# Performance work log

Hardware: AMD Instinct MI355X
Metric: run time of the kernel (lower is better)

The kernel has to match this reference:

```python
import jax, jax.numpy as jnp
import numpy as np

B, T, D = 2, 1024, 1024
H, DH = 16, 64
HD = H * DH          # head_dim = n_heads*d_head = 1024
F = 2048             # expert_dim
E = 8                # n_routed_experts


def bitlinear(x, W):
    # 1.58-bit ternary quant with straight-through estimator
    scale = jnp.clip(jnp.abs(W).mean(axis=1, keepdims=True), 1e-5, None)
    wq = jnp.clip(jnp.round(W / scale), -1.0, 1.0)
    w = W + jax.lax.stop_gradient(wq * scale - W)
    return x @ w.T


def layernorm(x, g, b):
    m = jnp.mean(x, -1, keepdims=True)
    v = jnp.mean((x - m) ** 2, -1, keepdims=True)
    return (x - m) * jax.lax.rsqrt(v + 1e-5) * g + b


def setup_inputs():
    key = jax.random.key(0)
    ks = jax.random.split(key, 12)
    n = lambda k, s, sd: jax.random.normal(k, s, jnp.float32) * sd
    return {
        'x': jax.random.normal(ks[0], (B, T, D), jnp.float32),
        'mask': jnp.tril(jnp.ones((T, T), bool))[None, None],  # causal [1,1,T,T]
        'Wq': n(ks[1], (2 * HD, D), (2 * HD) ** -0.5),
        'Wk': n(ks[2], (2 * HD, D), (2 * HD) ** -0.5),
        'Wv': n(ks[3], (HD, D), HD ** -0.5),
        'Wo': n(ks[4], (D, HD), D ** -0.5),
        'lambda_q': n(ks[5], (H, DH), 0.1),
        'lambda_k': n(ks[6], (H, DH), 0.1),
        'qn_g': jnp.ones(2 * HD), 'qn_b': jnp.zeros(2 * HD),
        'kn_g': jnp.ones(2 * HD), 'kn_b': jnp.zeros(2 * HD),
        'attn_g': jnp.ones(D), 'attn_b': jnp.zeros(D),
        'ffn_g': jnp.ones(D), 'ffn_b': jnp.zeros(D),
        'moe_g': jnp.ones(D), 'moe_b': jnp.zeros(D),
        'shared_w1': n(ks[7], (F, D), F ** -0.5),
        'shared_w2': n(ks[8], (D, F), D ** -0.5),
        'expert_w1': n(ks[9], (E, F, D), F ** -0.5),
        'expert_w2': n(ks[10], (E, D, F), D ** -0.5),
        'router_w': n(ks[11], (E, D), 0.02),
    }


def diff_attention(x, mask, Wq, Wk, Wv, Wo, lambda_q, lambda_k, qn_g, qn_b, kn_g, kn_b):
    Bq, Tq, _ = x.shape
    q = layernorm(bitlinear(x, Wq), qn_g, qn_b).reshape(Bq, Tq, 2, H, DH)
    k = layernorm(bitlinear(x, Wk), kn_g, kn_b).reshape(Bq, Tq, 2, H, DH)
    v = bitlinear(x, Wv).reshape(Bq, Tq, H, DH)
    lam = jnp.clip(jnp.exp(lambda_q.mean() - lambda_k.mean()), 0.1, 2.0)
    scale = DH ** -0.5

    def one_attn(qi, ki):
        s = jnp.einsum('bthd,bshd->bhts', qi, ki) * scale
        s = jnp.where(mask, s, -jnp.inf)
        p = jax.nn.softmax(s, -1)
        return jnp.einsum('bhts,bshd->bthd', p, v)

    out1 = one_attn(q[:, :, 0], k[:, :, 0])
    out2 = one_attn(q[:, :, 1], k[:, :, 1])
    out = (out1 - lam * out2).reshape(Bq, Tq, HD)
    return bitlinear(out, Wo)


def ignition_moe(x, moe_g, moe_b, shared_w1, shared_w2, expert_w1, expert_w2, router_w):
    h = layernorm(x, moe_g, moe_b)
    shared = bitlinear(jax.nn.silu(bitlinear(h, shared_w1)), shared_w2)
    probs = jax.nn.softmax(h @ router_w.T, -1)          # [B,T,E]
    idx = jnp.argmax(probs, -1)                          # top-1 expert id
    top_p = jnp.take_along_axis(probs, idx[..., None], -1)  # [B,T,1]
    routed = jnp.zeros_like(h)
    for e in range(E):  # small fixed expert count
        out_e = bitlinear(jax.nn.silu(bitlinear(h, expert_w1[e])), expert_w2[e])
        sel = (idx == e)[..., None]
        routed = routed + jnp.where(sel, out_e * top_p, 0.0)
    return shared + routed


def reference(x, mask, Wq, Wk, Wv, Wo, lambda_q, lambda_k, qn_g, qn_b, kn_g, kn_b,
              attn_g, attn_b, ffn_g, ffn_b, moe_g, moe_b,
              shared_w1, shared_w2, expert_w1, expert_w2, router_w):
    h = layernorm(x, attn_g, attn_b)
    x = x + diff_attention(h, mask, Wq, Wk, Wv, Wo, lambda_q, lambda_k, qn_g, qn_b, kn_g, kn_b)
    h = layernorm(x, ffn_g, ffn_b)
    x = x + ignition_moe(h, moe_g, moe_b, shared_w1, shared_w2, expert_w1, expert_w2, router_w)
    return x
```

## Files before the change

kernel.cpp:

```cpp
#include <hip/hip_runtime.h>
#include <hip/hip_bf16.h>

#define B_ 2
#define T_ 1024
#define D_ 1024
#define H_ 16
#define DH_ 64
#define F_ 2048
#define E_ 8
#define M_ 2048

typedef _Float16 half8 __attribute__((ext_vector_type(8)));
typedef _Float16 half4v __attribute__((ext_vector_type(4)));
typedef float f32x4 __attribute__((ext_vector_type(4)));

template<bool ABS>
__device__ __forceinline__ float np_pairwise_wave(const float* a, int K, int lane) {
  int nb = K >> 7;
  float s = 0.f;
  if (lane < nb) {
    const float* p = a + (lane << 7);
    float r[8];
    #pragma unroll
    for (int j = 0; j < 8; ++j) r[j] = ABS ? fabsf(p[j]) : p[j];
    for (int i = 8; i < 128; i += 8)
      #pragma unroll
      for (int j = 0; j < 8; ++j) r[j] += ABS ? fabsf(p[i + j]) : p[i + j];
    s = ((r[0] + r[1]) + (r[2] + r[3])) + ((r[4] + r[5]) + (r[6] + r[7]));
  }
  for (int off = 1; off < nb; off <<= 1) s += __shfl_xor(s, off);
  return __shfl(s, 0);
}

__global__ __launch_bounds__(64) void k_scaleq(const float* __restrict__ W, int K,
                                               float* __restrict__ scOut,
                                               _Float16* __restrict__ qOut) {
  int r = blockIdx.x, lane = threadIdx.x;
  const float* row = W + (size_t)r * K;
  float S = np_pairwise_wave<true>(row, K, lane);
  float s = fmaxf(S / (float)K, 1e-5f);
  if (lane == 0) scOut[r] = s;
  _Float16* dst = qOut + (size_t)r * K;
  for (int k = lane * 4; k < K; k += 256) {
    float4 w = *reinterpret_cast<const float4*>(row + k);
    float wv[4] = {w.x, w.y, w.z, w.w};
    half4v q4;
    #pragma unroll
    for (int j = 0; j < 4; ++j) {
      float q = rintf(wv[j] / s);
      q = fminf(1.f, fmaxf(-1.f, q));
      q4[j] = (_Float16)q;
    }
    *reinterpret_cast<half4v*>(dst + k) = q4;
  }
}

__global__ __launch_bounds__(64) void k_lambda(const float* __restrict__ lq,
                                               const float* __restrict__ lk,
                                               float* __restrict__ lam) {
  int lane = threadIdx.x;
  float mq = np_pairwise_wave<false>(lq, 1024, lane) / 1024.0f;
  float mk = np_pairwise_wave<false>(lk, 1024, lane) / 1024.0f;
  if (lane == 0) {
    float l = expf(mq - mk);
    lam[0] = fminf(2.0f, fmaxf(0.1f, l));
  }
}

__global__ __launch_bounds__(256) void k_layernorm(const float* __restrict__ in,
                                                   const float* __restrict__ g,
                                                   const float* __restrict__ b,
                                                   float* __restrict__ out, int Dd) {
  #pragma clang fp contract(off)
  __shared__ float row[2048];
  __shared__ float sq[2048];
  __shared__ float stat[2];
  int m = blockIdx.x, tid = threadIdx.x;
  const float* src = in + (size_t)m * Dd;
  for (int d = tid; d < Dd; d += 256) row[d] = src[d];
  __syncthreads();
  if (tid < 64) {
    float S = np_pairwise_wave<false>(row, Dd, tid);
    if (tid == 0) stat[0] = S;
  }
  __syncthreads();
  float mean = stat[0] / (float)Dd;
  for (int d = tid; d < Dd; d += 256) { float t = row[d] - mean; sq[d] = t * t; }
  __syncthreads();
  if (tid < 64) {
    float S = np_pairwise_wave<false>(sq, Dd, tid);
    if (tid == 0) stat[1] = S;
  }
  __syncthreads();
  float var = stat[1] / (float)Dd;
  float rs = 1.0f / sqrtf(var + 1e-5f);
  float* dst = out + (size_t)m * Dd;
  for (int d = tid; d < Dd; d += 256) {
    float t = row[d] - mean;
    float u = t * rs;
    float v = u * g[d];
    dst[d] = v + b[d];
  }
}

__global__ __launch_bounds__(256) void k_layernorm_split(const float* __restrict__ in,
                                                         const float* __restrict__ g,
                                                         const float* __restrict__ b,
                                                         _Float16* __restrict__ oh,
                                                         _Float16* __restrict__ ol, int Dd) {
  #pragma clang fp contract(off)
  __shared__ float row[2048];
  __shared__ float sq[2048];
  __shared__ float stat[2];
  int m = blockIdx.x, tid = threadIdx.x;
  const float* src = in + (size_t)m * Dd;
  for (int d = tid; d < Dd; d += 256) row[d] = src[d];
  __syncthreads();
  if (tid < 64) {
    float S = np_pairwise_wave<false>(row, Dd, tid);
    if (tid == 0) stat[0] = S;
  }
  __syncthreads();
  float mean = stat[0] / (float)Dd;
  for (int d = tid; d < Dd; d += 256) { float t = row[d] - mean; sq[d] = t * t; }
  __syncthreads();
  if (tid < 64) {
    float S = np_pairwise_wave<false>(sq, Dd, tid);
    if (tid == 0) stat[1] = S;
  }
  __syncthreads();
  float var = stat[1] / (float)Dd;
  float rs = 1.0f / sqrtf(var + 1e-5f);
  #pragma unroll 1
  for (int d = tid; d < Dd; d += 256) {
    float t = row[d] - mean;
    float u = t * rs;
    float v = u * g[d];
    float w = v + b[d];
    _Float16 hv = (_Float16)w;
    oh[(size_t)m * Dd + d] = hv;
    ol[(size_t)m * Dd + d] = (_Float16)((w - (float)hv) * 2048.0f);
  }
}

__global__ __launch_bounds__(256) void k_lnln(const float* __restrict__ in,
                                              const float* __restrict__ g1, const float* __restrict__ b1,
                                              const float* __restrict__ g2, const float* __restrict__ b2,
                                              float* __restrict__ outf,
                                              _Float16* __restrict__ outh) {
  #pragma clang fp contract(off)
  __shared__ float row[1024];
  __shared__ float tmp[1024];
  __shared__ float stat[2];
  int m = blockIdx.x, tid = threadIdx.x;
  const float* src = in + (size_t)m * 1024;
  for (int d = tid; d < 1024; d += 256) row[d] = src[d];
  __syncthreads();
  if (tid < 64) { float S = np_pairwise_wave<false>(row, 1024, tid); if (tid == 0) stat[0] = S; }
  __syncthreads();
  float mean = stat[0] / 1024.0f;
  for (int d = tid; d < 1024; d += 256) { float t = row[d] - mean; tmp[d] = t * t; }
  __syncthreads();
  if (tid < 64) { float S = np_pairwise_wave<false>(tmp, 1024, tid); if (tid == 0) stat[1] = S; }
  __syncthreads();
  float rs = 1.0f / sqrtf(stat[1] / 1024.0f + 1e-5f);
  for (int d = tid; d < 1024; d += 256) {
    float t = row[d] - mean;
    float u = t * rs;
    float v = u * g1[d];
    tmp[d] = v + b1[d];
  }
  __syncthreads();
  if (tid < 64) { float S = np_pairwise_wave<false>(tmp, 1024, tid); if (tid == 0) stat[0] = S; }
  __syncthreads();
  float mean2 = stat[0] / 1024.0f;
  for (int d = tid; d < 1024; d += 256) { float t = tmp[d] - mean2; row[d] = t * t; }
  __syncthreads();
  if (tid < 64) { float S = np_pairwise_wave<false>(row, 1024, tid); if (tid == 0) stat[1] = S; }
  __syncthreads();
  float rs2 = 1.0f / sqrtf(stat[1] / 1024.0f + 1e-5f);
  for (int d = tid; d < 1024; d += 256) {
    float t = tmp[d] - mean2;
    float u = t * rs2;
    float v = u * g2[d];
    float w = v + b2[d];
    outf[(size_t)m * 1024 + d] = w;
    outh[(size_t)m * 1024 + d] = (_Float16)w;
  }
}

template<int EPI, int XM, int DUAL>
__global__ __launch_bounds__(256) void k_mgemm(
    const _Float16* __restrict__ Agh, const _Float16* __restrict__ Agl, int lda,
    const _Float16* __restrict__ Wh, const float* __restrict__ scf,
    float* __restrict__ Cout, _Float16* __restrict__ Ch, _Float16* __restrict__ Ch2,
    int ldc, int N, int K,
    const float* __restrict__ res, const float* __restrict__ add2,
    const int* __restrict__ offs, const int* __restrict__ tlist,
    const float* __restrict__ topp)
{
  int e = XM ? blockIdx.z : 0;
  int mbase = 0, mcount = M_;
  const float* sc = scf;
  const _Float16* Whb = Wh;
  if (XM) {
    mbase = offs[e]; mcount = offs[e + 1] - mbase;
    Whb = Wh + (size_t)e * N * K;
    sc = scf + (size_t)e * N;
  }
  int m0 = blockIdx.y * 128;
  if (XM && m0 >= mcount) return;
  int n0 = blockIdx.x * 64;

  __shared__ __align__(16) _Float16 As[4][128][8];
  __shared__ __align__(16) _Float16 Als[DUAL ? 4 : 1][128][8];
  __shared__ __align__(16) _Float16 Qs[4][64][8];

  int tid = threadIdx.x;
  int lm  = tid >> 1;
  int kcA = (tid & 1) * 16;
  int lw  = tid >> 2;
  int kcW = (tid & 3) * 8;

  int am  = m0 + lm;
  int amc = XM ? ((am < mcount) ? am : (mcount - 1)) : am;
  int arow;
  if (XM == 1)      arow = tlist[mbase + amc];
  else if (XM == 2) arow = mbase + amc;
  else              arow = am;
  const _Float16* Arh = Agh + (size_t)arow * lda;
  const _Float16* Arl = DUAL ? (Agl + (size_t)arow * lda) : nullptr;
  const _Float16* Wrh = Whb + (size_t)(n0 + lw) * K;

  int wv = tid >> 6, lane = tid & 63;
  int wm = wv >> 1, wn = wv & 1;
  int ks = lane >> 4, fr = lane & 15;

  f32x4 acch[4][2], accl[4][2];
  #pragma unroll
  for (int i = 0; i < 4; i++)
    #pragma unroll
    for (int j = 0; j < 2; j++) { acch[i][j] = (f32x4)0.f; accl[i][j] = (f32x4)0.f; }

  for (int kt = 0; kt < K; kt += 32) {
    half8 a0 = *reinterpret_cast<const half8*>(Arh + kt + kcA);
    half8 a1 = *reinterpret_cast<const half8*>(Arh + kt + kcA + 8);
    half8 b0, b1;
    if (DUAL) {
      b0 = *reinterpret_cast<const half8*>(Arl + kt + kcA);
      b1 = *reinterpret_cast<const half8*>(Arl + kt + kcA + 8);
    }
    half8 qv = *reinterpret_cast<const half8*>(Wrh + kt + kcW);
    __syncthreads();
    int sA = kcA >> 3;
    *reinterpret_cast<half8*>(&As[sA][lm][0])     = a0;
    *reinterpret_cast<half8*>(&As[sA + 1][lm][0]) = a1;
    if (DUAL) {
      *reinterpret_cast<half8*>(&Als[sA][lm][0])     = b0;
      *reinterpret_cast<half8*>(&Als[sA + 1][lm][0]) = b1;
    }
    *reinterpret_cast<half8*>(&Qs[kcW >> 3][lw][0]) = qv;
    __syncthreads();
    half8 bfr0 = *reinterpret_cast<half8*>(&Qs[ks][wn * 32 + fr][0]);
    half8 bfr1 = *reinterpret_cast<half8*>(&Qs[ks][wn * 32 + 16 + fr][0]);
    #pragma unroll
    for (int i = 0; i < 4; i++) {
      half8 ah = *reinterpret_cast<half8*>(&As[ks][wm * 64 + i * 16 + fr][0]);
      acch[i][0] = __builtin_amdgcn_mfma_f32_16x16x32_f16(ah, bfr0, acch[i][0], 0, 0, 0);
      acch[i][1] = __builtin_amdgcn_mfma_f32_16x16x32_f16(ah, bfr1, acch[i][1], 0, 0, 0);
      if (DUAL) {
        half8 al = *reinterpret_cast<half8*>(&Als[ks][wm * 64 + i * 16 + fr][0]);
        accl[i][0] = __builtin_amdgcn_mfma_f32_16x16x32_f16(al, bfr0, accl[i][0], 0, 0, 0);
        accl[i][1] = __builtin_amdgcn_mfma_f32_16x16x32_f16(al, bfr1, accl[i][1], 0, 0, 0);
      }
    }
  }

  #pragma unroll
  for (int j = 0; j < 2; j++) {
    int col = n0 + wn * 32 + j * 16 + fr;
    float scl = sc[col];
    #pragma unroll
    for (int i = 0; i < 4; i++) {
      #pragma unroll
      for (int r = 0; r < 4; r++) {
        int lrow = m0 + wm * 64 + i * 16 + ks * 4 + r;
        if (XM && lrow >= mcount) continue;
        int orow;
        if (XM == 1)      orow = mbase + lrow;
        else if (XM == 2) orow = tlist[mbase + lrow];
        else              orow = lrow;
        float v = acch[i][j][r];
        if (DUAL) v += accl[i][j][r] * (1.0f / 2048.0f);
        v *= scl;
        if (EPI == 1) {
          v = v * (1.0f / (1.0f + expf(-v)));
          Ch[(size_t)orow * ldc + col] = (_Float16)v;
        } else if (EPI == 3) {
          float rt = v * topp[orow];
          float moe = add2[(size_t)orow * ldc + col] + rt;
          Cout[(size_t)orow * ldc + col] = res[(size_t)orow * ldc + col] + moe;
        } else if (EPI == 5) {
          int bb = orow >> 10, tok = orow & 1023;
          size_t vidx = ((size_t)(bb << 10) + col) * 1024 + tok;
          _Float16 hv = (_Float16)v;
          Ch[vidx] = hv;
          Ch2[vidx] = (_Float16)((v - (float)hv) * 2048.0f);
        } else if (EPI == 2) {
          Cout[(size_t)orow * ldc + col] = res[(size_t)orow * ldc + col] + v;
        } else {
          Cout[(size_t)orow * ldc + col] = v;
        }
      }
    }
  }
}

__global__ __launch_bounds__(256) void k_mgemm_qkv(
    const _Float16* __restrict__ Agh, const _Float16* __restrict__ Agl,
    const _Float16* __restrict__ WQ_, const _Float16* __restrict__ WK_, const _Float16* __restrict__ WV_,
    const float* __restrict__ scq, const float* __restrict__ sck, const float* __restrict__ scv,
    float* __restrict__ Cq, float* __restrict__ Ck,
    _Float16* __restrict__ Vth, _Float16* __restrict__ Vtl)
{
  int nt = blockIdx.x;
  int sel = (nt < 32) ? 0 : (nt < 64 ? 1 : 2);
  int n0 = ((sel == 0) ? nt : (sel == 1) ? (nt - 32) : (nt - 64)) * 64;
  const _Float16* Wh = (sel == 0) ? WQ_ : (sel == 1) ? WK_ : WV_;
  const float* sc = (sel == 0) ? scq : (sel == 1) ? sck : scv;
  int m0 = blockIdx.y * 128;

  __shared__ __align__(16) _Float16 As[4][128][8];
  __shared__ __align__(16) _Float16 Als[4][128][8];
  __shared__ __align__(16) _Float16 Qs[4][64][8];

  int tid = threadIdx.x;
  int lm  = tid >> 1;
  int kcA = (tid & 1) * 16;
  int lw  = tid >> 2;
  int kcW = (tid & 3) * 8;

  const _Float16* Arh = Agh + (size_t)(m0 + lm) * 1024;
  const _Float16* Arl = Agl + (size_t)(m0 + lm) * 1024;
  const _Float16* Wrh = Wh + (size_t)(n0 + lw) * 1024;

  int wv = tid >> 6, lane = tid & 63;
  int wm = wv >> 1, wn = wv & 1;
  int ks = lane >> 4, fr = lane & 15;

  f32x4 acch[4][2], accl[4][2];
  #pragma unroll
  for (int i = 0; i < 4; i++)
    #pragma unroll
    for (int j = 0; j < 2; j++) { acch[i][j] = (f32x4)0.f; accl[i][j] = (f32x4)0.f; }

  for (int kt = 0; kt < 1024; kt += 32) {
    half8 a0 = *reinterpret_cast<const half8*>(Arh + kt + kcA);
    half8 a1 = *reinterpret_cast<const half8*>(Arh + kt + kcA + 8);
    half8 b0 = *reinterpret_cast<const half8*>(Arl + kt + kcA);
    half8 b1 = *reinterpret_cast<const half8*>(Arl + kt + kcA + 8);
    half8 qv = *reinterpret_cast<const half8*>(Wrh + kt + kcW);
    __syncthreads();
    int sA = kcA >> 3;
    *reinterpret_cast<half8*>(&As[sA][lm][0])      = a0;
    *reinterpret_cast<half8*>(&As[sA + 1][lm][0])  = a1;
    *reinterpret_cast<half8*>(&Als[sA][lm][0])     = b0;
    *reinterpret_cast<half8*>(&Als[sA + 1][lm][0]) = b1;
    *reinterpret_cast<half8*>(&Qs[kcW >> 3][lw][0]) = qv;
    __syncthreads();
    half8 bfr0 = *reinterpret_cast<half8*>(&Qs[ks][wn * 32 + fr][0]);
    half8 bfr1 = *reinterpret_cast<half8*>(&Qs[ks][wn * 32 + 16 + fr][0]);
    #pragma unroll
    for (int i = 0; i < 4; i++) {
      half8 ah = *reinterpret_cast<half8*>(&As[ks][wm * 64 + i * 16 + fr][0]);
      half8 al = *reinterpret_cast<half8*>(&Als[ks][wm * 64 + i * 16 + fr][0]);
      acch[i][0] = __builtin_amdgcn_mfma_f32_16x16x32_f16(ah, bfr0, acch[i][0], 0, 0, 0);
      acch[i][1] = __builtin_amdgcn_mfma_f32_16x16x32_f16(ah, bfr1, acch[i][1], 0, 0, 0);
      accl[i][0] = __builtin_amdgcn_mfma_f32_16x16x32_f16(al, bfr0, accl[i][0], 0, 0, 0);
      accl[i][1] = __builtin_amdgcn_mfma_f32_16x16x32_f16(al, bfr1, accl[i][1], 0, 0, 0);
    }
  }

  #pragma unroll
  for (int j = 0; j < 2; j++) {
    int col = n0 + wn * 32 + j * 16 + fr;
    float scl = sc[col];
    #pragma unroll
    for (int i = 0; i < 4; i++) {
      #pragma unroll
      for (int r = 0; r < 4; r++) {
        int orow = m0 + wm * 64 + i * 16 + ks * 4 + r;
        float v = (acch[i][j][r] + accl[i][j][r] * (1.0f / 2048.0f)) * scl;
        if (sel == 0) {
          Cq[(size_t)orow * 2048 + col] = v;
        } else if (sel == 1) {
          Ck[(size_t)orow * 2048 + col] = v;
        } else {
          int bb = orow >> 10, tok = orow & 1023;
          size_t vidx = ((size_t)(bb << 10) + col) * 1024 + tok;
          _Float16 hv = (_Float16)v;
          Vth[vidx] = hv;
          Vtl[vidx] = (_Float16)((v - (float)hv) * 2048.0f);
        }
      }
    }
  }
}

__global__ __launch_bounds__(256) void k_mgemm_moe1(
    const _Float16* __restrict__ Agh,
    const _Float16* __restrict__ WhS, const _Float16* __restrict__ WhE,
    const float* __restrict__ scS, const float* __restrict__ scE,
    _Float16* __restrict__ CS, _Float16* __restrict__ CE,
    const int* __restrict__ offs, const int* __restrict__ tlist)
{
  int z = blockIdx.z;
  int mbase = 0, mcount = M_;
  const _Float16* Whb = WhS;
  const float* sc = scS;
  if (z > 0) {
    int e = z - 1;
    mbase = offs[e]; mcount = offs[e + 1] - mbase;
    Whb = WhE + (size_t)e * 2048 * 1024;
    sc = scE + (size_t)e * 2048;
  }
  int m0 = blockIdx.y * 128;
  if (z > 0 && m0 >= mcount) return;
  int n0 = blockIdx.x * 64;

  __shared__ __align__(16) _Float16 As[4][128][8];
  __shared__ __align__(16) _Float16 Qs[4][64][8];

  int tid = threadIdx.x;
  int lm  = tid >> 1;
  int kcA = (tid & 1) * 16;
  int lw  = tid >> 2;
  int kcW = (tid & 3) * 8;

  int am  = m0 + lm;
  int amc = (z > 0) ? ((am < mcount) ? am : (mcount - 1)) : am;
  int arow = (z > 0) ? tlist[mbase + amc] : am;
  const _Float16* Arh = Agh + (size_t)arow * 1024;
  const _Float16* Wrh = Whb + (size_t)(n0 + lw) * 1024;

  int wv = tid >> 6, lane = tid & 63;
  int wm = wv >> 1, wn = wv & 1;
  int ks = lane >> 4, fr = lane & 15;

  f32x4 acch[4][2];
  #pragma unroll
  for (int i = 0; i < 4; i++)
    #pragma unroll
    for (int j = 0; j < 2; j++) acch[i][j] = (f32x4)0.f;

  for (int kt = 0; kt < 1024; kt += 32) {
    half8 a0 = *reinterpret_cast<const half8*>(Arh + kt + kcA);
    half8 a1 = *reinterpret_cast<const half8*>(Arh + kt + kcA + 8);
    half8 qv = *reinterpret_cast<const half8*>(Wrh + kt + kcW);
    __syncthreads();
    int sA = kcA >> 3;
    *reinterpret_cast<half8*>(&As[sA][lm][0])     = a0;
    *reinterpret_cast<half8*>(&As[sA + 1][lm][0]) = a1;
    *reinterpret_cast<half8*>(&Qs[kcW >> 3][lw][0]) = qv;
    __syncthreads();
    half8 bfr0 = *reinterpret_cast<half8*>(&Qs[ks][wn * 32 + fr][0]);
    half8 bfr1 = *reinterpret_cast<half8*>(&Qs[ks][wn * 32 + 16 + fr][0]);
    #pragma unroll
    for (int i = 0; i < 4; i++) {
      half8 ah = *reinterpret_cast<half8*>(&As[ks][wm * 64 + i * 16 + fr][0]);
      acch[i][0] = __builtin_amdgcn_mfma_f32_16x16x32_f16(ah, bfr0, acch[i][0], 0, 0, 0);
      acch[i][1] = __builtin_amdgcn_mfma_f32_16x16x32_f16(ah, bfr1, acch[i][1], 0, 0, 0);
    }
  }

  #pragma unroll
  for (int j = 0; j < 2; j++) {
    int col = n0 + wn * 32 + j * 16 + fr;
    float scl = sc[col];
    #pragma unroll
    for (int i = 0; i < 4; i++) {
      #pragma unroll
      for (int r = 0; r < 4; r++) {
        int lrow = m0 + wm * 64 + i * 16 + ks * 4 + r;
        if (z > 0 && lrow >= mcount) continue;
        float v = acch[i][j][r] * scl;
        v = v * (1.0f / (1.0f + expf(-v)));
        if (z > 0) CE[(size_t)(mbase + lrow) * 2048 + col] = (_Float16)v;
        else       CS[(size_t)lrow * 2048 + col] = (_Float16)v;
      }
    }
  }
}

__global__ __launch_bounds__(256) void k_attn4(const float* __restrict__ q,
                                               const _Float16* __restrict__ khg,
                                               const _Float16* __restrict__ klg,
                                               const _Float16* __restrict__ vth,
                                               const _Float16* __restrict__ vtl,
                                               const float* __restrict__ lamp,
                                               _Float16* __restrict__ aoh,
                                               _Float16* __restrict__ aol)
{
  __shared__ __align__(16) _Float16 KH[2][64][72];
  __shared__ __align__(16) _Float16 KL[2][64][72];
  __shared__ __align__(16) _Float16 VH[64][72];
  __shared__ __align__(16) _Float16 VL[64][72];
  __shared__ __align__(16) _Float16 PH[4][16][72];
  __shared__ __align__(16) _Float16 PL[4][16][72];

  int bh = blockIdx.x;
  int b = bh >> 4, h = bh & 15;
  int y = blockIdx.y;
  int tq = (y < 8) ? (2 * y) : (31 - 2 * y);
  int t0 = tq * 64;
  int tid = threadIdx.x;
  int wm = tid >> 6, lane = tid & 63;
  int ks = lane >> 4, fr = lane & 15;
  size_t tokbase = (size_t)b * T_;
  float lam = lamp[0];

  half8 qh[2][2], ql[2][2];
  {
    const float* qr = q + (tokbase + t0 + wm * 16 + fr) * 2048 + h * 64;
    #pragma unroll
    for (int g = 0; g < 2; ++g)
      #pragma unroll
      for (int s = 0; s < 2; ++s) {
        const float* p = qr + g * 1024 + s * 32 + ks * 8;
        float4 x0 = *reinterpret_cast<const float4*>(p);
        float4 x1 = *reinterpret_cast<const float4*>(p + 4);
        float xv[8] = {x0.x,x0.y,x0.z,x0.w, x1.x,x1.y,x1.z,x1.w};
        half8 hh, ll;
        #pragma unroll
        for (int j = 0; j < 8; ++j) {
          _Float16 hv = (_Float16)xv[j];
          hh[j] = hv; ll[j] = (_Float16)((xv[j] - (float)hv) * 2048.0f);
        }
        qh[g][s] = hh; ql[g][s] = ll;
      }
  }

  f32x4 Oh[2][4], Ox[2][4];
  #pragma unroll
  for (int g = 0; g < 2; ++g)
    #pragma unroll
    for (int d = 0; d < 4; ++d) { Oh[g][d] = (f32x4)0.f; Ox[g][d] = (f32x4)0.f; }
  float mrun[2][4], lrun[2][4];
  #pragma unroll
  for (int g = 0; g < 2; ++g)
    #pragma unroll
    for (int r = 0; r < 4; ++r) { mrun[g][r] = -1e30f; lrun[g][r] = 0.f; }

  for (int jt = 0; jt <= tq; ++jt) {
    int kv0 = jt * 64;
    __syncthreads();
    {
      int key = tid & 63;
      int d0 = (tid >> 6) * 16;
      #pragma unroll
      for (int g = 0; g < 2; ++g) {
        const _Float16* sh = khg + ((size_t)(tokbase + kv0 + key)) * 2048 + g * 1024 + h * 64 + d0;
        const _Float16* sl = klg + ((size_t)(tokbase + kv0 + key)) * 2048 + g * 1024 + h * 64 + d0;
        *reinterpret_cast<half8*>(&KH[g][key][d0])     = *reinterpret_cast<const half8*>(sh);
        *reinterpret_cast<half8*>(&KH[g][key][d0 + 8]) = *reinterpret_cast<const half8*>(sh + 8);
        *reinterpret_cast<half8*>(&KL[g][key][d0])     = *reinterpret_cast<const half8*>(sl);
        *reinterpret_cast<half8*>(&KL[g][key][d0 + 8]) = *reinterpret_cast<const half8*>(sl + 8);
      }
      int dd = tid & 63;
      int k0 = (tid >> 6) * 16;
      size_t vb = ((size_t)b * 1024 + h * 64 + dd) * 1024 + kv0 + k0;
      *reinterpret_cast<half8*>(&VH[dd][k0])     = *reinterpret_cast<const half8*>(vth + vb);
      *reinterpret_cast<half8*>(&VH[dd][k0 + 8]) = *reinterpret_cast<const half8*>(vth + vb + 8);
      *reinterpret_cast<half8*>(&VL[dd][k0])     = *reinterpret_cast<const half8*>(vtl + vb);
      *reinterpret_cast<half8*>(&VL[dd][k0 + 8]) = *reinterpret_cast<const half8*>(vtl + vb + 8);
    }
    __syncthreads();

    bool diag = (jt == tq);
    #pragma unroll
    for (int g = 0; g < 2; ++g) {
      f32x4 Sh[4], Sx[4];
      #pragma unroll
      for (int kf = 0; kf < 4; ++kf) { Sh[kf] = (f32x4)0.f; Sx[kf] = (f32x4)0.f; }
      #pragma unroll
      for (int s = 0; s < 2; ++s) {
        #pragma unroll
        for (int kf = 0; kf < 4; ++kf) {
          half8 kh = *reinterpret_cast<half8*>(&KH[g][kf * 16 + fr][s * 32 + ks * 8]);
          half8 kl = *reinterpret_cast<half8*>(&KL[g][kf * 16 + fr][s * 32 + ks * 8]);
          Sh[kf] = __builtin_amdgcn_mfma_f32_16x16x32_f16(qh[g][s], kh, Sh[kf], 0, 0, 0);
          Sx[kf] = __builtin_amdgcn_mfma_f32_16x16x32_f16(qh[g][s], kl, Sx[kf], 0, 0, 0);
          Sx[kf] = __builtin_amdgcn_mfma_f32_16x16x32_f16(ql[g][s], kh, Sx[kf], 0, 0, 0);
        }
      }
      float sv[4][4];
      #pragma unroll
      for (int kf = 0; kf < 4; ++kf)
        #pragma unroll
        for (int r = 0; r < 4; ++r) {
          float s_ = (Sh[kf][r] + Sx[kf][r] * (1.0f / 2048.0f)) * 0.125f;
          if (diag) {
            int row_abs = t0 + wm * 16 + ks * 4 + r;
            int col_abs = kv0 + kf * 16 + fr;
            if (col_abs > row_abs) s_ = -1e30f;
          }
          sv[kf][r] = s_;
        }
      #pragma unroll
      for (int r = 0; r < 4; ++r) {
        float tmax = fmaxf(fmaxf(sv[0][r], sv[1][r]), fmaxf(sv[2][r], sv[3][r]));
        #pragma unroll
        for (int msk = 1; msk < 16; msk <<= 1) tmax = fmaxf(tmax, __shfl_xor(tmax, msk));
        bool up = tmax > mrun[g][r];
        float mnew = up ? tmax : mrun[g][r];
        float e0 = expf(sv[0][r] - mnew);
        float e1 = expf(sv[1][r] - mnew);
        float e2 = expf(sv[2][r] - mnew);
        float e3 = expf(sv[3][r] - mnew);
        float rsum = (e0 + e1) + (e2 + e3);
        #pragma unroll
        for (int msk = 1; msk < 16; msk <<= 1) rsum += __shfl_xor(rsum, msk);
        if (up) {
          float scale = expf(mrun[g][r] - tmax);
          lrun[g][r] = lrun[g][r] * scale + rsum;
          mrun[g][r] = tmax;
          #pragma unroll
          for (int df = 0; df < 4; ++df) { Oh[g][df][r] *= scale; Ox[g][df][r] *= scale; }
        } else {
          lrun[g][r] += rsum;
        }
        float ev[4] = {e0, e1, e2, e3};
        #pragma unroll
        for (int kf = 0; kf < 4; ++kf) {
          _Float16 ph = (_Float16)ev[kf];
          _Float16 pl = (_Float16)((ev[kf] - (float)ph) * 2048.0f);
          PH[wm][ks * 4 + r][kf * 16 + fr] = ph;
          PL[wm][ks * 4 + r][kf * 16 + fr] = pl;
        }
      }
      #pragma unroll
      for (int s = 0; s < 2; ++s) {
        half8 pah = *reinterpret_cast<half8*>(&PH[wm][fr][s * 32 + ks * 8]);
        half8 pal = *reinterpret_cast<half8*>(&PL[wm][fr][s * 32 + ks * 8]);
        #pragma unroll
        for (int df = 0; df < 4; ++df) {
          half8 vh = *reinterpret_cast<half8*>(&VH[df * 16 + fr][s * 32 + ks * 8]);
          half8 vl = *reinterpret_cast<half8*>(&VL[df * 16 + fr][s * 32 + ks * 8]);
          Oh[g][df] = __builtin_amdgcn_mfma_f32_16x16x32_f16(pah, vh, Oh[g][df], 0, 0, 0);
          Ox[g][df] = __builtin_amdgcn_mfma_f32_16x16x32_f16(pah, vl, Ox[g][df], 0, 0, 0);
          Ox[g][df] = __builtin_amdgcn_mfma_f32_16x16x32_f16(pal, vh, Ox[g][df], 0, 0, 0);
        }
      }
    }
  }

  #pragma unroll
  for (int df = 0; df < 4; ++df) {
    #pragma unroll
    for (int r = 0; r < 4; ++r) {
      int row_abs = t0 + wm * 16 + ks * 4 + r;
      int d = df * 16 + fr;
      float o1 = (Oh[0][df][r] + Ox[0][df][r] * (1.0f / 2048.0f)) / lrun[0][r];
      float o2 = (Oh[1][df][r] + Ox[1][df][r] * (1.0f / 2048.0f)) / lrun[1][r];
      float oo = o1 - lam * o2;
      size_t idx = (tokbase + row_abs) * 1024 + h * 64 + d;
      _Float16 hv = (_Float16)oo;
      aoh[idx] = hv;
      aol[idx] = (_Float16)((oo - (float)hv) * 2048.0f);
    }
  }
}

__global__ __launch_bounds__(256) void k_router(const float* __restrict__ hm,
                                                const float* __restrict__ rw,
                                                int* __restrict__ idx,
                                                float* __restrict__ topp)
{
  #pragma clang fp contract(off)
  int tid = threadIdx.x;
  int tg = tid >> 3, e = tid & 7;
  int m = blockIdx.x * 32 + tg;
  const float* hr = hm + (size_t)m * 1024;
  const float* wr = rw + (size_t)e * 1024;
  float l = 0.f;
  for (int dd = 0; dd < 1024; ++dd) l = __builtin_fmaf(hr[dd], wr[dd], l);
  float mx = l;
  #pragma unroll
  for (int off = 1; off < 8; off <<= 1) mx = fmaxf(mx, __shfl_xor(mx, off, 8));
  float p = expf(l - mx);
  float den = p;
  #pragma unroll
  for (int off = 1; off < 8; off <<= 1) den += __shfl_xor(den, off, 8);
  float prob = p / den;
  float pm = prob;
  #pragma unroll
  for (int off = 1; off < 8; off <<= 1) pm = fmaxf(pm, __shfl_xor(pm, off, 8));
  unsigned long long ball = __ballot(prob == pm);
  int grp = (tid & 63) >> 3;
  int first = __ffsll((unsigned long long)((ball >> (grp * 8)) & 0xFFull)) - 1;
  if (e == 0) { idx[m] = first; topp[m] = pm; }
}

__global__ __launch_bounds__(512) void k_route_fill(const int* __restrict__ idx,
                                                    int* __restrict__ offs,
                                                    int* __restrict__ tlist)
{
  __shared__ int cnt[8];
  __shared__ int off[9];
  int w = threadIdx.x >> 6, lane = threadIdx.x & 63;
  int total = 0;
  for (int it = 0; it < M_ / 64; ++it) {
    int tok = it * 64 + lane;
    unsigned long long m = __ballot(idx[tok] == w);
    total += __popcll(m);
  }
  if (lane == 0) cnt[w] = total;
  __syncthreads();
  if (threadIdx.x == 0) {
    int o = 0;
    for (int e = 0; e < 8; ++e) { off[e] = o; o += cnt[e]; }
    off[8] = o;
    for (int e = 0; e < 9; ++e) offs[e] = off[e];
  }
  __syncthreads();
  int base = off[w];
  for (int it = 0; it < M_ / 64; ++it) {
    int tok = it * 64 + lane;
    bool sel = (idx[tok] == w);
    unsigned long long m = __ballot(sel);
    if (sel) {
      int pos = base + __popcll(m & ((1ull << lane) - 1ull));
      tlist[pos] = tok;
    }
    base += __popcll(m);
  }
}

extern "C" void kernel_launch(void* const* d_in, const int* in_sizes, int n_in,
                              void* d_out, int out_size, void* d_ws, size_t ws_size,
                              hipStream_t stream) {
  const float* x   = (const float*)d_in[0];
  const float* Wq  = (const float*)d_in[2];
  const float* Wk  = (const float*)d_in[3];
  const float* Wv  = (const float*)d_in[4];
  const float* Wo  = (const float*)d_in[5];
  const float* lq  = (const float*)d_in[6];
  const float* lk  = (const float*)d_in[7];
  const float* qng = (const float*)d_in[8];
  const float* qnb = (const float*)d_in[9];
  const float* kng = (const float*)d_in[10];
  const float* knb = (const float*)d_in[11];
  const float* ag  = (const float*)d_in[12];
  const float* ab  = (const float*)d_in[13];
  const float* fg  = (const float*)d_in[14];
  const float* fb  = (const float*)d_in[15];
  const float* mg  = (const float*)d_in[16];
  const float* mb  = (const float*)d_in[17];
  const float* sw1 = (const float*)d_in[18];
  const float* sw2 = (const float*)d_in[19];
  const float* ew1 = (const float*)d_in[20];
  const float* ew2 = (const float*)d_in[21];
  const float* rw  = (const float*)d_in[22];

  float* ws = (float*)d_ws;
  size_t o = 0;
  float* scWq = ws + o; o += 2048;
  float* scWk = ws + o; o += 2048;
  float* scWv = ws + o; o += 1024;
  float* scWo = ws + o; o += 1024;
  float* scS1 = ws + o; o += 2048;
  float* scS2 = ws + o; o += 1024;
  float* scE1 = ws + o; o += 8 * 2048;
  float* scE2 = ws + o; o += 8 * 1024;
  float* lam  = ws + o; o += 16;
  float* TOPP = ws + o; o += 2048;
  int*   IDX  = (int*)(ws + o); o += 2048;
  int*   OFFS = (int*)(ws + o); o += 16;
  int*   TLIST= (int*)(ws + o); o += 2048;
  o = (o + 15) & ~(size_t)15;

  _Float16* QWq = (_Float16*)(ws + o); o += 1024 * 1024;
  _Float16* QWk = (_Float16*)(ws + o); o += 1024 * 1024;
  _Float16* QWv = (_Float16*)(ws + o); o += 512 * 1024;
  _Float16* QWo = (_Float16*)(ws + o); o += 512 * 1024;
  _Float16* QS1 = (_Float16*)(ws + o); o += 1024 * 1024;
  _Float16* QS2 = (_Float16*)(ws + o); o += 1024 * 1024;
  _Float16* QE1 = (_Float16*)(ws + o); o += 8 * 1024 * 1024;
  _Float16* QE2 = (_Float16*)(ws + o); o += 8 * 1024 * 1024;

  float* RA = ws + o; o += 2 * 1024 * 1024;
  _Float16* H1h = (_Float16*)RA;
  _Float16* H1l = (_Float16*)(RA + 1024 * 1024);
  _Float16* SMh = (_Float16*)RA;
  float* RB = ws + o; o += 2 * 1024 * 1024;
  _Float16* AOh = (_Float16*)RB;
  _Float16* AOl = (_Float16*)(RB + 1024 * 1024);
  _Float16* HMh = (_Float16*)RB;
  _Float16* T1h = (_Float16*)(ws + o); o += 2 * 1024 * 1024;

  const size_t MQ = (size_t)M_ * 2048;
  float* QP = ws + o; o += MQ;
  float* KP = ws + o; o += MQ;
  _Float16* KHg = (_Float16*)(ws + o); o += 2 * 1024 * 1024;
  _Float16* KLg = (_Float16*)(ws + o); o += 2 * 1024 * 1024;
  _Float16* VTH = (_Float16*)(ws + o); o += 1024 * 1024;
  _Float16* VTL = (_Float16*)(ws + o); o += 1024 * 1024;

  float* X1 = QP;
  float* HM = QP + MQ / 2;
  float* SO = KP;

  k_scaleq<<<2048, 64, 0, stream>>>(Wq,  1024, scWq, QWq);
  k_scaleq<<<2048, 64, 0, stream>>>(Wk,  1024, scWk, QWk);
  k_scaleq<<<1024, 64, 0, stream>>>(Wv,  1024, scWv, QWv);
  k_scaleq<<<1024, 64, 0, stream>>>(Wo,  1024, scWo, QWo);
  k_scaleq<<<2048, 64, 0, stream>>>(sw1, 1024, scS1, QS1);
  k_scaleq<<<1024, 64, 0, stream>>>(sw2, 2048, scS2, QS2);
  k_scaleq<<<8 * 2048, 64, 0, stream>>>(ew1, 1024, scE1, QE1);
  k_scaleq<<<8 * 1024, 64, 0, stream>>>(ew2, 2048, scE2, QE2);
  k_lambda<<<1, 64, 0, stream>>>(lq, lk, lam);

  k_layernorm_split<<<M_, 256, 0, stream>>>(x, ag, ab, H1h, H1l, 1024);
  k_mgemm_qkv<<<dim3(80,16), 256, 0, stream>>>(H1h, H1l, QWq, QWk, QWv, scWq, scWk, scWv, QP, KP, VTH, VTL);
  k_layernorm<<<M_, 256, 0, stream>>>(QP, qng, qnb, QP, 2048);
  k_layernorm_split<<<M_, 256, 0, stream>>>(KP, kng, knb, KHg, KLg, 2048);
  k_attn4<<<dim3(32, 16), 256, 0, stream>>>(QP, KHg, KLg, VTH, VTL, lam, AOh, AOl);
  k_mgemm<2,0,1><<<dim3(16,16), 256, 0, stream>>>(AOh, AOl, 1024, QWo, scWo, X1, nullptr, nullptr, 1024, 1024, 1024, x, nullptr, nullptr, nullptr, nullptr);

  k_lnln<<<M_, 256, 0, stream>>>(X1, fg, fb, mg, mb, HM, HMh);
  k_router<<<M_ / 32, 256, 0, stream>>>(HM, rw, IDX, TOPP);
  k_route_fill<<<1, 512, 0, stream>>>(IDX, OFFS, TLIST);

  k_mgemm_moe1<<<dim3(32,16,9), 256, 0, stream>>>(HMh, QS1, QE1, scS1, scE1, SMh, T1h, OFFS, TLIST);

  k_mgemm<0,0,0><<<dim3(16,16), 256, 0, stream>>>(SMh, nullptr, 2048, QS2, scS2, SO, nullptr, nullptr, 1024, 1024, 2048, nullptr, nullptr, nullptr, nullptr, nullptr);
  k_mgemm<3,2,0><<<dim3(16,16,8), 256, 0, stream>>>(T1h, nullptr, 2048, QE2, scE2, (float*)d_out, nullptr, nullptr, 1024, 1024, 2048, X1, SO, OFFS, TLIST, TOPP);
}
```

Before: 653.2 us.

## Merge weight quant launches, fuse MoE second GEMMs, prefetch attention tiles, fast exp

All eight per-weight ternary quantization launches become one kernel that picks the weight by block index. The shared and routed second-layer MoE GEMMs run in one grid, and a separate elementwise kernel then adds the residual. The attention kernel now prefetches the next K/V tile into registers while the current tile is processed. expf is replaced by __expf throughout. This cuts launch overhead, lets the two MoE GEMMs run concurrently, and hides load latency. In exchange it adds an extra elementwise pass, raises register pressure in attention, and uses a less precise exp.

```diff
diff --git a/kernel.cpp b/kernel.cpp
--- a/kernel.cpp
+++ b/kernel.cpp
@@ -32,15 +32,35 @@
   return __shfl(s, 0);
 }
 
-__global__ __launch_bounds__(64) void k_scaleq(const float* __restrict__ W, int K,
-                                               float* __restrict__ scOut,
-                                               _Float16* __restrict__ qOut) {
+__global__ __launch_bounds__(64) void k_scaleq_all(
+    const float* __restrict__ Wq, const float* __restrict__ Wk,
+    const float* __restrict__ Wv, const float* __restrict__ Wo,
+    const float* __restrict__ sw1, const float* __restrict__ sw2,
+    const float* __restrict__ ew1, const float* __restrict__ ew2,
+    float* __restrict__ scWq, float* __restrict__ scWk,
+    float* __restrict__ scWv, float* __restrict__ scWo,
+    float* __restrict__ scS1, float* __restrict__ scS2,
+    float* __restrict__ scE1, float* __restrict__ scE2,
+    _Float16* __restrict__ QWq, _Float16* __restrict__ QWk,
+    _Float16* __restrict__ QWv, _Float16* __restrict__ QWo,
+    _Float16* __restrict__ QS1, _Float16* __restrict__ QS2,
+    _Float16* __restrict__ QE1, _Float16* __restrict__ QE2)
+{
   int r = blockIdx.x, lane = threadIdx.x;
-  const float* row = W + (size_t)r * K;
+  const float* W; float* sc; _Float16* qo; int K; int rr;
+  if      (r < 2048)  { W = Wq;  sc = scWq; qo = QWq; K = 1024; rr = r; }
+  else if (r < 4096)  { W = Wk;  sc = scWk; qo = QWk; K = 1024; rr = r - 2048; }
+  else if (r < 5120)  { W = Wv;  sc = scWv; qo = QWv; K = 1024; rr = r - 4096; }
+  else if (r < 6144)  { W = Wo;  sc = scWo; qo = QWo; K = 1024; rr = r - 5120; }
+  else if (r < 8192)  { W = sw1; sc = scS1; qo = QS1; K = 1024; rr = r - 6144; }
+  else if (r < 9216)  { W = sw2; sc = scS2; qo = QS2; K = 2048; rr = r - 8192; }
+  else if (r < 25600) { W = ew1; sc = scE1; qo = QE1; K = 1024; rr = r - 9216; }
+  else                { W = ew2; sc = scE2; qo = QE2; K = 2048; rr = r - 25600; }
+  const float* row = W + (size_t)rr * K;
   float S = np_pairwise_wave<true>(row, K, lane);
   float s = fmaxf(S / (float)K, 1e-5f);
-  if (lane == 0) scOut[r] = s;
-  _Float16* dst = qOut + (size_t)r * K;
+  if (lane == 0) sc[rr] = s;
+  _Float16* dst = qo + (size_t)rr * K;
   for (int k = lane * 4; k < K; k += 256) {
     float4 w = *reinterpret_cast<const float4*>(row + k);
     float wv[4] = {w.x, w.y, w.z, w.w};
@@ -294,18 +314,8 @@
         if (DUAL) v += accl[i][j][r] * (1.0f / 2048.0f);
         v *= scl;
         if (EPI == 1) {
-          v = v * (1.0f / (1.0f + expf(-v)));
+          v = v * (1.0f / (1.0f + __expf(-v)));
           Ch[(size_t)orow * ldc + col] = (_Float16)v;
-        } else if (EPI == 3) {
-          float rt = v * topp[orow];
-          float moe = add2[(size_t)orow * ldc + col] + rt;
-          Cout[(size_t)orow * ldc + col] = res[(size_t)orow * ldc + col] + moe;
-        } else if (EPI == 5) {
-          int bb = orow >> 10, tok = orow & 1023;
-          size_t vidx = ((size_t)(bb << 10) + col) * 1024 + tok;
-          _Float16 hv = (_Float16)v;
-          Ch[vidx] = hv;
-          Ch2[vidx] = (_Float16)((v - (float)hv) * 2048.0f);
         } else if (EPI == 2) {
           Cout[(size_t)orow * ldc + col] = res[(size_t)orow * ldc + col] + v;
         } else {
@@ -484,12 +494,113 @@
         int lrow = m0 + wm * 64 + i * 16 + ks * 4 + r;
         if (z > 0 && lrow >= mcount) continue;
         float v = acch[i][j][r] * scl;
-        v = v * (1.0f / (1.0f + expf(-v)));
+        v = v * (1.0f / (1.0f + __expf(-v)));
         if (z > 0) CE[(size_t)(mbase + lrow) * 2048 + col] = (_Float16)v;
         else       CS[(size_t)lrow * 2048 + col] = (_Float16)v;
       }
     }
   }
+}
+
+__global__ __launch_bounds__(256) void k_mgemm_moe2(
+    const _Float16* __restrict__ SMh, const _Float16* __restrict__ T1h,
+    const _Float16* __restrict__ WhS, const _Float16* __restrict__ WhE,
+    const float* __restrict__ scS, const float* __restrict__ scE,
+    float* __restrict__ SO, float* __restrict__ RT,
+    const int* __restrict__ offs, const int* __restrict__ tlist,
+    const float* __restrict__ topp)
+{
+  int z = blockIdx.z;
+  int mbase = 0, mcount = M_;
+  const _Float16* Agh = SMh;
+  const _Float16* Whb = WhS;
+  const float* sc = scS;
+  if (z > 0) {
+    int e = z - 1;
+    mbase = offs[e]; mcount = offs[e + 1] - mbase;
+    Agh = T1h;
+    Whb = WhE + (size_t)e * 1024 * 2048;
+    sc = scE + (size_t)e * 1024;
+  }
+  int m0 = blockIdx.y * 128;
+  if (z > 0 && m0 >= mcount) return;
+  int n0 = blockIdx.x * 64;
+
+  __shared__ __align__(16) _Float16 As[4][128][8];
+  __shared__ __align__(16) _Float16 Qs[4][64][8];
+
+  int tid = threadIdx.x;
+  int lm  = tid >> 1;
+  int kcA = (tid & 1) * 16;
+  int lw  = tid >> 2;
+  int kcW = (tid & 3) * 8;
+
+  int am  = m0 + lm;
+  int amc = (z > 0) ? ((am < mcount) ? am : (mcount - 1)) : am;
+  int arow = (z > 0) ? (mbase + amc) : am;
+  const _Float16* Arh = Agh + (size_t)arow * 2048;
+  const _Float16* Wrh = Whb + (size_t)(n0 + lw) * 2048;
+
+  int wv = tid >> 6, lane = tid & 63;
+  int wm = wv >> 1, wn = wv & 1;
+  int ks = lane >> 4, fr = lane & 15;
+
+  f32x4 acch[4][2];
+  #pragma unroll
+  for (int i = 0; i < 4; i++)
+    #pragma unroll
+    for (int j = 0; j < 2; j++) acch[i][j] = (f32x4)0.f;
+
+  for (int kt = 0; kt < 2048; kt += 32) {
+    half8 a0 = *reinterpret_cast<const half8*>(Arh + kt + kcA);
+    half8 a1 = *reinterpret_cast<const half8*>(Arh + kt + kcA + 8);
+    half8 qv = *reinterpret_cast<const half8*>(Wrh + kt + kcW);
+    __syncthreads();
+    int sA = kcA >> 3;
+    *reinterpret_cast<half8*>(&As[sA][lm][0])     = a0;
+    *reinterpret_cast<half8*>(&As[sA + 1][lm][0]) = a1;
+    *reinterpret_cast<half8*>(&Qs[kcW >> 3][lw][0]) = qv;
+    __syncthreads();
+    half8 bfr0 = *reinterpret_cast<half8*>(&Qs[ks][wn * 32 + fr][0]);
+    half8 bfr1 = *reinterpret_cast<half8*>(&Qs[ks][wn * 32 + 16 + fr][0]);
+    #pragma unroll
+    for (int i = 0; i < 4; i++) {
+      half8 ah = *reinterpret_cast<half8*>(&As[ks][wm * 64 + i * 16 + fr][0]);
+      acch[i][0] = __builtin_amdgcn_mfma_f32_16x16x32_f16(ah, bfr0, acch[i][0], 0, 0, 0);
+      acch[i][1] = __builtin_amdgcn_mfma_f32_16x16x32_f16(ah, bfr1, acch[i][1], 0, 0, 0);
+    }
+  }
+
+  #pragma unroll
+  for (int j = 0; j < 2; j++) {
+    int col = n0 + wn * 32 + j * 16 + fr;
+    float scl = sc[col];
+    #pragma unroll
+    for (int i = 0; i < 4; i++) {
+      #pragma unroll
+      for (int r = 0; r < 4; r++) {
+        int lrow = m0 + wm * 64 + i * 16 + ks * 4 + r;
+        if (z > 0 && lrow >= mcount) continue;
+        float v = acch[i][j][r] * scl;
+        if (z > 0) {
+          int orow = tlist[mbase + lrow];
+          RT[(size_t)orow * 1024 + col] = v * topp[orow];
+        } else {
+          SO[(size_t)lrow * 1024 + col] = v;
+        }
+      }
+    }
+  }
+}
+
+__global__ __launch_bounds__(256) void k_final(const float* __restrict__ x1,
+                                               const float* __restrict__ so,
+                                               const float* __restrict__ rt,
+                                               float* __restrict__ out) {
+  #pragma clang fp contract(off)
+  int i = blockIdx.x * 256 + threadIdx.x;
+  float moe = so[i] + rt[i];
+  out[i] = x1[i] + moe;
 }
 
 __global__ __launch_bounds__(256) void k_attn4(const float* __restrict__ q,
@@ -551,28 +662,56 @@
     #pragma unroll
     for (int r = 0; r < 4; ++r) { mrun[g][r] = -1e30f; lrun[g][r] = 0.f; }
 
+  int key = tid & 63;
+  int d0 = (tid >> 6) * 16;
+  half8 rkh[2][2], rkl[2][2], rvh[2], rvl[2];
+  {
+    #pragma unroll
+    for (int g = 0; g < 2; ++g) {
+      const _Float16* sh = khg + (size_t)(tokbase + key) * 2048 + g * 1024 + h * 64 + d0;
+      const _Float16* sl = klg + (size_t)(tokbase + key) * 2048 + g * 1024 + h * 64 + d0;
+      rkh[g][0] = *reinterpret_cast<const half8*>(sh);
+      rkh[g][1] = *reinterpret_cast<const half8*>(sh + 8);
+      rkl[g][0] = *reinterpret_cast<const half8*>(sl);
+      rkl[g][1] = *reinterpret_cast<const half8*>(sl + 8);
+    }
+    size_t vb = ((size_t)b * 1024 + h * 64 + key) * 1024 + d0;
+    rvh[0] = *reinterpret_cast<const half8*>(vth + vb);
+    rvh[1] = *reinterpret_cast<const half8*>(vth + vb + 8);
+    rvl[0] = *reinterpret_cast<const half8*>(vtl + vb);
+    rvl[1] = *reinterpret_cast<const half8*>(vtl + vb + 8);
+  }
+
   for (int jt = 0; jt <= tq; ++jt) {
     int kv0 = jt * 64;
     __syncthreads();
-    {
-      int key = tid & 63;
-      int d0 = (tid >> 6) * 16;
+    #pragma unroll
+    for (int g = 0; g < 2; ++g) {
+      *reinterpret_cast<half8*>(&KH[g][key][d0])     = rkh[g][0];
+      *reinterpret_cast<half8*>(&KH[g][key][d0 + 8]) = rkh[g][1];
+      *reinterpret_cast<half8*>(&KL[g][key][d0])     = rkl[g][0];
+      *reinterpret_cast<half8*>(&KL[g][key][d0 + 8]) = rkl[g][1];
+    }
+    *reinterpret_cast<half8*>(&VH[key][d0])     = rvh[0];
+    *reinterpret_cast<half8*>(&VH[key][d0 + 8]) = rvh[1];
+    *reinterpret_cast<half8*>(&VL[key][d0])     = rvl[0];
+    *reinterpret_cast<half8*>(&VL[key][d0 + 8]) = rvl[1];
+    if (jt < tq) {
+      int nv0 = kv0 + 64;
       #pragma unroll
       for (int g = 0; g < 2; ++g) {
-        const _Float16* sh = khg + ((size_t)(tokbase + kv0 + key)) * 2048 + g * 1024 + h * 64 + d0;
-        const _Float16* sl = klg + ((size_t)(tokbase + kv0 + key)) * 2048 + g * 1024 + h * 64 + d0;
-        *reinterpret_cast<half8*>(&KH[g][key][d0])     = *reinterpret_cast<const half8*>(sh);
-        *reinterpret_cast<half8*>(&KH[g][key][d0 + 8]) = *reinterpret_cast<const half8*>(sh + 8);
-        *reinterpret_cast<half8*>(&KL[g][key][d0])     = *reinterpret_cast<const half8*>(sl);
-        *reinterpret_cast<half8*>(&KL[g][key][d0 + 8]) = *reinterpret_cast<const half8*>(sl + 8);
+        const _Float16* sh = khg + (size_t)(tokbase + nv0 + key) * 2048 + g * 1024 + h * 64 + d0;
+        const _Float16* sl = klg + (size_t)(tokbase + nv0 + key) * 2048 + g * 1024 + h * 64 + d0;
+        rkh[g][0] = *reinterpret_cast<const half8*>(sh);
+        rkh[g][1] = *reinterpret_cast<const half8*>(sh + 8);
+        rkl[g][0] = *reinterpret_cast<const half8*>(sl);
+        rkl[g][1] = *reinterpret_cast<const half8*>(sl + 8);
       }
-      int dd = tid & 63;
-      int k0 = (tid >> 6) * 16;
-      size_t vb = ((size_t)b * 1024 + h * 64 + dd) * 1024 + kv0 + k0;
-      *reinterpret_cast<half8*>(&VH[dd][k0])     = *reinterpret_cast<const half8*>(vth + vb);
-      *reinterpret_cast<half8*>(&VH[dd][k0 + 8]) = *reinterpret_cast<const half8*>(vth + vb + 8);
-      *reinterpret_cast<half8*>(&VL[dd][k0])     = *reinterpret_cast<const half8*>(vtl + vb);
-      *reinterpret_cast<half8*>(&VL[dd][k0 + 8]) = *reinterpret_cast<const half8*>(vtl + vb + 8);
+      size_t vb = ((size_t)b * 1024 + h * 64 + key) * 1024 + nv0 + d0;
+      rvh[0] = *reinterpret_cast<const half8*>(vth + vb);
+      rvh[1] = *reinterpret_cast<const half8*>(vth + vb + 8);
+      rvl[0] = *reinterpret_cast<const half8*>(vtl + vb);
+      rvl[1] = *reinterpret_cast<const half8*>(vtl + vb + 8);
     }
     __syncthreads();
 
@@ -613,15 +752,15 @@
         for (int msk = 1; msk < 16; msk <<= 1) tmax = fmaxf(tmax, __shfl_xor(tmax, msk));
         bool up = tmax > mrun[g][r];
         float mnew = up ? tmax : mrun[g][r];
-        float e0 = expf(sv[0][r] - mnew);
-        float e1 = expf(sv[1][r] - mnew);
-        float e2 = expf(sv[2][r] - mnew);
-        float e3 = expf(sv[3][r] - mnew);
+        float e0 = __expf(sv[0][r] - mnew);
+        float e1 = __expf(sv[1][r] - mnew);
+        float e2 = __expf(sv[2][r] - mnew);
+        float e3 = __expf(sv[3][r] - mnew);
         float rsum = (e0 + e1) + (e2 + e3);
         #pragma unroll
         for (int msk = 1; msk < 16; msk <<= 1) rsum += __shfl_xor(rsum, msk);
         if (up) {
-          float scale = expf(mrun[g][r] - tmax);
+          float scale = __expf(mrun[g][r] - tmax);
           lrun[g][r] = lrun[g][r] * scale + rsum;
           mrun[g][r] = tmax;
           #pragma unroll
@@ -687,7 +826,7 @@
   float mx = l;
   #pragma unroll
   for (int off = 1; off < 8; off <<= 1) mx = fmaxf(mx, __shfl_xor(mx, off, 8));
-  float p = expf(l - mx);
+  float p = __expf(l - mx);
   float den = p;
   #pragma unroll
   for (int off = 1; off < 8; off <<= 1) den += __shfl_xor(den, off, 8);
@@ -809,15 +948,11 @@
   float* X1 = QP;
   float* HM = QP + MQ / 2;
   float* SO = KP;
-
-  k_scaleq<<<2048, 64, 0, stream>>>(Wq,  1024, scWq, QWq);
-  k_scaleq<<<2048, 64, 0, stream>>>(Wk,  1024, scWk, QWk);
-  k_scaleq<<<1024, 64, 0, stream>>>(Wv,  1024, scWv, QWv);
-  k_scaleq<<<1024, 64, 0, stream>>>(Wo,  1024, scWo, QWo);
-  k_scaleq<<<2048, 64, 0, stream>>>(sw1, 1024, scS1, QS1);
-  k_scaleq<<<1024, 64, 0, stream>>>(sw2, 2048, scS2, QS2);
-  k_scaleq<<<8 * 2048, 64, 0, stream>>>(ew1, 1024, scE1, QE1);
-  k_scaleq<<<8 * 1024, 64, 0, stream>>>(ew2, 2048, scE2, QE2);
+  float* RT = (float*)KHg;
+
+  k_scaleq_all<<<33792, 64, 0, stream>>>(Wq, Wk, Wv, Wo, sw1, sw2, ew1, ew2,
+                                         scWq, scWk, scWv, scWo, scS1, scS2, scE1, scE2,
+                                         QWq, QWk, QWv, QWo, QS1, QS2, QE1, QE2);
   k_lambda<<<1, 64, 0, stream>>>(lq, lk, lam);
 
   k_layernorm_split<<<M_, 256, 0, stream>>>(x, ag, ab, H1h, H1l, 1024);
@@ -832,7 +967,7 @@
   k_route_fill<<<1, 512, 0, stream>>>(IDX, OFFS, TLIST);
 
   k_mgemm_moe1<<<dim3(32,16,9), 256, 0, stream>>>(HMh, QS1, QE1, scS1, scE1, SMh, T1h, OFFS, TLIST);
-
-  k_mgemm<0,0,0><<<dim3(16,16), 256, 0, stream>>>(SMh, nullptr, 2048, QS2, scS2, SO, nullptr, nullptr, 1024, 1024, 2048, nullptr, nullptr, nullptr, nullptr, nullptr);
-  k_mgemm<3,2,0><<<dim3(16,16,8), 256, 0, stream>>>(T1h, nullptr, 2048, QE2, scE2, (float*)d_out, nullptr, nullptr, 1024, 1024, 2048, X1, SO, OFFS, TLIST, TOPP);
-}
+  k_mgemm_moe2<<<dim3(16,16,9), 256, 0, stream>>>(SMh, T1h, QS2, QE2, scS2, scE2, SO, RT, OFFS, TLIST, TOPP);
+
+  k_final<<<8192, 256, 0, stream>>>(X1, SO, RT, (float*)d_out);
+}
```

Result: faster. 539.8 us (-17.4%).
